# Performance work log

Hardware: AMD Instinct MI355X
Metric: run time of the kernel (lower is better)

The kernel has to match this reference:

```python
import jax, jax.numpy as jnp
import numpy as np

N, S, C, P, K = 64, 64, 128, 32, 1000   # batch, frames, in_planes, part_num, class_num
HPG = (3 * C) // 16                      # hidden channels per group for part_score mlp = 24
EPS = 1e-5


def setup_inputs() -> dict:
    key = jax.random.key(0)
    ks = jax.random.split(key, 8)
    return {
        "t_f": jax.random.normal(ks[0], (N, S, C, P), jnp.float32),
        "t_s": jax.random.normal(ks[1], (N, S, C, P), jnp.float32),
        "t_l": jax.random.normal(ks[2], (N, S, C, P), jnp.float32),
        # part_score grouped 1x1 convs (groups=P): per-group (out, in)
        "w1": jax.random.normal(ks[3], (P, HPG, 3 * C), jnp.float32) * 0.05,
        "bn1_gamma": jnp.ones((P, HPG), jnp.float32),
        "bn1_beta": jnp.zeros((P, HPG), jnp.float32),
        "w2": jax.random.normal(ks[4], (P, 1, HPG), jnp.float32) * 0.05,
        # decay_channel grouped 1x1 conv: per-group 3C -> C
        "wd": jax.random.normal(ks[5], (P, C, 3 * C), jnp.float32) * 0.05,
        # per-part BatchNorm1d(C) affine params
        "bn_gamma": jnp.ones((P, C), jnp.float32),
        "bn_beta": jnp.zeros((P, C), jnp.float32),
        # fc: (1, C, K) in torch; squeeze leading 1
        "fc": jax.random.normal(ks[6], (C, K), jnp.float32) * 0.05,
    }


def reference(t_f, t_s, t_l, w1, bn1_gamma, bn1_beta, w2, wd, bn_gamma, bn_beta, fc):
    # cat along channel dim then arrange as (n, p, 3c, s) == grouped conv layout
    x = jnp.concatenate([t_f, t_s, t_l], axis=2).transpose(0, 3, 2, 1)  # (n,p,3c,s)

    # --- part_score: grouped 1x1 conv -> BN (batch stats over n,s) -> LeakyReLU -> grouped conv -> sigmoid
    h = jnp.einsum('npis,poi->npos', x, w1)               # (n,p,HPG,s)
    mu = h.mean(axis=(0, 3), keepdims=True)
    var = h.var(axis=(0, 3), keepdims=True)               # biased var (torch training BN)
    h = (h - mu) / jnp.sqrt(var + EPS) * bn1_gamma[None, :, :, None] + bn1_beta[None, :, :, None]
    h = jnp.where(h >= 0, h, 0.01 * h)                    # LeakyReLU(0.01)
    score = jax.nn.sigmoid(jnp.einsum('npis,poi->npos', h, w2))  # (n,p,1,s)

    # --- decay_channel grouped 1x1 conv: 3c -> c per part
    feat = jnp.einsum('npis,poi->npos', x, wd)            # (n,p,c,s)

    # attention-weighted temporal pooling
    wpv = (feat * score).sum(-1) / score.sum(-1)          # (n,p,c)

    # per-part BatchNorm1d over batch dim (training-mode batch stats)
    m = wpv.mean(axis=0)                                  # (p,c)
    v = wpv.var(axis=0)
    part_feature = ((wpv - m) / jnp.sqrt(v + EPS) * bn_gamma + bn_beta).transpose(1, 0, 2)  # (p,n,c)

    part_classification = jnp.einsum('pnc,ck->pnk', part_feature, fc)  # (p,n,K)

    # argmax frame per (n,p) and gather from t_f
    idx = jnp.argmax(score[:, :, 0, :], axis=-1)          # (n,p)
    tfp = t_f.transpose(0, 3, 1, 2)                       # (n,p,s,c)
    selected = jnp.take_along_axis(tfp, idx[:, :, None, None], axis=2)[:, :, 0, :]  # (n,p,c)
    selected_part_feature = selected.transpose(1, 0, 2)   # (p,n,c)

    weighted_part_vector = wpv.transpose(1, 0, 2)         # (p,n,c)
    return part_classification, weighted_part_vector, selected_part_feature
```

## Files before the change

### kernel.cpp

```cpp
#include <hip/hip_runtime.h>
#include <math.h>

#define N 64
#define S 64
#define C 128
#define P 32
#define KCLS 1000
#define HPG 24
#define C3 384
#define NS 4096
#define EPSV 1e-5f

#define WS_H    0
#define WS_W1Z  (WS_H + P*HPG*NS)
#define WS_BNP  (WS_W1Z + 384*8*32*4)
#define WS_BNSS (WS_BNP + 512*768*2)
#define WS_Y    (WS_BNSS + P*HPG*2)
#define WS_Z    (WS_Y + P*N*C3)
#define WS_PF   (WS_Z + P*N)
#define WS_SC   (WS_PF + P*C*N)
#define WS_MI   (WS_SC + N*P*S)

__global__ __launch_bounds__(256) void k0w_w1z(
    const float* __restrict__ w1, float* __restrict__ w1z)
{
  int e = blockIdx.x * 256 + threadIdx.x;
  int p = e & 31;
  int og = (e >> 5) & 7;
  int i = e >> 8;
  float4 v;
  v.x = w1[(p * HPG + og * 3 + 0) * C3 + i];
  v.y = w1[(p * HPG + og * 3 + 1) * C3 + i];
  v.z = w1[(p * HPG + og * 3 + 2) * C3 + i];
  v.w = 0.f;
  ((float4*)w1z)[e] = v;
}

__global__ __launch_bounds__(256) void k01_h(
    const float* __restrict__ tf, const float* __restrict__ ts,
    const float* __restrict__ tl, const float* __restrict__ w1z,
    float* __restrict__ h, float* __restrict__ bnpT)
{
  int n = blockIdx.x, st = blockIdx.y;
  int s0 = st * 8;
  int t = threadIdx.x;
  int p = t & 31;
  int og = t >> 5;
  __shared__ float xl[8 * 1024];
  float acc[3][8];
  #pragma unroll
  for (int oo = 0; oo < 3; ++oo)
    #pragma unroll
    for (int s = 0; s < 8; ++s) acc[oo][s] = 0.f;

  const float4* w4p = (const float4*)w1z;
  const float* xp = &xl[p];
  for (int ch = 0; ch < 12; ++ch) {
    int z = ch >> 2, c0 = (ch & 3) * 32;
    const float* src = (z == 0) ? tf : (z == 1) ? ts : tl;
    const float* base = src + ((size_t)(n * S + s0)) * C * P + c0 * P;
    if (ch) __syncthreads();
    #pragma unroll
    for (int j = 0; j < 8; ++j) {
      int e = t + 256 * j;
      int s_loc = e >> 8;
      int idx = e & 255;
      float4 v = *(const float4*)&base[(size_t)s_loc * C * P + idx * 4];
      *(float4*)&xl[s_loc * 1024 + idx * 4] = v;
    }
    __syncthreads();
    #pragma unroll 4
    for (int cl = 0; cl < 32; ++cl) {
      int i = ch * 32 + cl;
      float4 w = w4p[(i * 8 + og) * 32 + p];
      float xs[8];
      #pragma unroll
      for (int s = 0; s < 8; ++s) xs[s] = xp[s * 1024 + cl * 32];
      #pragma unroll
      for (int s = 0; s < 8; ++s) {
        acc[0][s] += w.x * xs[s];
        acc[1][s] += w.y * xs[s];
        acc[2][s] += w.z * xs[s];
      }
    }
  }
  int nst = n * 8 + st;
  #pragma unroll
  for (int oo = 0; oo < 3; ++oo) {
    int o = og * 3 + oo;
    float* hp = h + (size_t)(p * HPG + o) * NS + n * S + s0;
    *(float4*)&hp[0] = make_float4(acc[oo][0], acc[oo][1], acc[oo][2], acc[oo][3]);
    *(float4*)&hp[4] = make_float4(acc[oo][4], acc[oo][5], acc[oo][6], acc[oo][7]);
    float sm = 0.f, sq = 0.f;
    #pragma unroll
    for (int s = 0; s < 8; ++s) { sm += acc[oo][s]; sq += acc[oo][s] * acc[oo][s]; }
    bnpT[(size_t)((p * HPG + o) * 2 + 0) * 512 + nst] = sm;
    bnpT[(size_t)((p * HPG + o) * 2 + 1) * 512 + nst] = sq;
  }
}

__global__ __launch_bounds__(256) void k2_bnstat(const float* __restrict__ bnpT,
    const float* __restrict__ g, const float* __restrict__ b,
    float* __restrict__ bnss)
{
  int blk = blockIdx.x;
  int t = threadIdx.x;
  int rl = t >> 4, lane = t & 15;
  int row = blk * 16 + rl;
  const float* rp = bnpT + (size_t)row * 512;
  float sm = 0.f;
  #pragma unroll 8
  for (int j = 0; j < 32; ++j) sm += rp[lane + 16 * j];
  __shared__ float red[16][17];
  red[rl][lane] = sm;
  __syncthreads();
  if (t < 16) {
    float s = 0.f;
    #pragma unroll
    for (int j = 0; j < 16; ++j) s += red[t][j];
    red[t][16] = s;
  }
  __syncthreads();
  if (t < 8) {
    int po = blk * 8 + t;
    float sum = red[t * 2][16];
    float sq  = red[t * 2 + 1][16];
    float mu  = sum / (float)NS;
    float var = sq / (float)NS - mu * mu;
    float sc = g[po] * rsqrtf(var + EPSV);
    bnss[po * 2]     = sc;
    bnss[po * 2 + 1] = b[po] - mu * sc;
  }
}

__global__ __launch_bounds__(256) void k3a_score(
    const float* __restrict__ h, const float* __restrict__ bnss,
    const float* __restrict__ w2,
    float* __restrict__ score, float* __restrict__ z,
    int* __restrict__ mi_out)
{
  int n = blockIdx.x;
  int p = blockIdx.y * 4 + (threadIdx.x >> 6);
  int l = threadIdx.x & 63;
  float ssum = 0.f;
  const float* hp = h + (size_t)p * HPG * NS + n * S;
  #pragma unroll
  for (int o = 0; o < HPG; ++o) {
    float hv = hp[(size_t)o * NS + l];
    float sc = bnss[(p * HPG + o) * 2];
    float sh = bnss[(p * HPG + o) * 2 + 1];
    float v = hv * sc + sh;
    v = (v >= 0.f) ? v : 0.01f * v;
    ssum += w2[p * HPG + o] * v;
  }
  float scr = 1.f / (1.f + expf(-ssum));
  float zs = scr;
  #pragma unroll
  for (int m = 1; m < 64; m <<= 1) zs += __shfl_xor(zs, m, 64);
  float mv = scr; int mi = l;
  #pragma unroll
  for (int m = 1; m < 64; m <<= 1) {
    float ov = __shfl_xor(mv, m, 64);
    int   oi = __shfl_xor(mi, m, 64);
    if (ov > mv || (ov == mv && oi < mi)) { mv = ov; mi = oi; }
  }
  if (l == 0) { z[p * N + n] = zs; mi_out[n * P + p] = mi; }
  score[((size_t)n * P + p) * S + l] = scr;
}

__global__ __launch_bounds__(256) void k3b_y(
    const float* __restrict__ tf, const float* __restrict__ ts,
    const float* __restrict__ tl, const float* __restrict__ score,
    const int* __restrict__ mi, float* __restrict__ y,
    float* __restrict__ out_spf)
{
  int n = blockIdx.x, chunk = blockIdx.y;
  int z = chunk >> 2, c0 = (chunk & 3) * 32;
  const float* src = (z == 0) ? tf : (z == 1) ? ts : tl;
  int t = threadIdx.x;
  int p = t & 31, cl = t >> 5;
  __shared__ float sc_lds[S * P];
  __shared__ int mi_lds[P];
  #pragma unroll
  for (int j = 0; j < 8; ++j) {
    int e = t + 256 * j;
    int s2 = e >> 5, pp = e & 31;
    sc_lds[s2 * P + pp] = score[((size_t)n * P + pp) * S + s2];
  }
  if (t < P) mi_lds[t] = mi[n * P + t];
  __syncthreads();
  int mymi = mi_lds[p];
  const float* base = src + (size_t)n * S * C * P + (size_t)(c0 + cl) * P + p;
  float acc[4] = {0.f, 0.f, 0.f, 0.f};
  float sel[4] = {0.f, 0.f, 0.f, 0.f};
  #pragma unroll 8
  for (int s = 0; s < S; ++s) {
    float scv = sc_lds[s * P + p];
    #pragma unroll
    for (int j = 0; j < 4; ++j) {
      float v = base[(size_t)s * C * P + j * 8 * P];
      acc[j] += v * scv;
      sel[j] = (s == mymi) ? v : sel[j];
    }
  }
  float* yp = y + ((size_t)p * N + n) * C3 + z * C + c0 + cl;
  #pragma unroll
  for (int j = 0; j < 4; ++j) yp[j * 8] = acc[j];
  if (z == 0) {
    float* sp = out_spf + ((size_t)p * N + n) * C + c0 + cl;
    #pragma unroll
    for (int j = 0; j < 4; ++j) sp[j * 8] = sel[j];
  }
}

__global__ __launch_bounds__(256) void k4_wpv(
    const float* __restrict__ y, const float* __restrict__ z,
    const float* __restrict__ wd, const float* __restrict__ g,
    const float* __restrict__ b, float* __restrict__ out_wpv,
    float* __restrict__ pf)
{
  int p   = blockIdx.x;
  int cch = blockIdx.y;
  int t = threadIdx.x;
  int n = t & 63, cg = t >> 6;
  int cbase = cch * 16 + cg * 4;
  __shared__ float ych[96][66];
  float acc[4] = {0.f, 0.f, 0.f, 0.f};
  const float* yp  = y  + (size_t)p * N * C3;
  const float* wdp = wd + (size_t)p * C * C3;
  for (int ch = 0; ch < 4; ++ch) {
    __syncthreads();
    #pragma unroll
    for (int j = 0; j < 24; ++j) {
      int e = t + 256 * j;
      int i = e % 96, nn = e / 96;
      ych[i][nn] = yp[nn * C3 + ch * 96 + i];
    }
    __syncthreads();
    #pragma unroll
    for (int sub = 0; sub < 4; ++sub) {
      float yr[24];
      #pragma unroll
      for (int kk = 0; kk < 24; ++kk) yr[kk] = ych[sub * 24 + kk][n];
      int ibase = ch * 96 + sub * 24;
      #pragma unroll
      for (int cl = 0; cl < 4; ++cl) {
        const float4* w4 = (const float4*)(wdp + (size_t)(cbase + cl) * C3 + ibase);
        float a = 0.f;
        #pragma unroll
        for (int q = 0; q < 6; ++q) {
          float4 wv = w4[q];
          a += yr[q*4+0] * wv.x + yr[q*4+1] * wv.y
             + yr[q*4+2] * wv.z + yr[q*4+3] * wv.w;
        }
        acc[cl] += a;
      }
    }
  }
  float zinv = 1.f / z[p * N + n];
  #pragma unroll
  for (int cl = 0; cl < 4; ++cl) acc[cl] *= zinv;
  #pragma unroll
  for (int cl = 0; cl < 4; ++cl) {
    float v = acc[cl];
    float s = v, q = v * v;
    #pragma unroll
    for (int m = 1; m < 64; m <<= 1) {
      s += __shfl_xor(s, m, 64);
      q += __shfl_xor(q, m, 64);
    }
    float mu  = s * (1.f / 64.f);
    float var = q * (1.f / 64.f) - mu * mu;
    int c = cbase + cl;
    float sc = g[p * C + c] * rsqrtf(var + EPSV);
    float sh = b[p * C + c] - mu * sc;
    pf[((size_t)p * C + c) * N + n] = v * sc + sh;
  }
  float4 wout = make_float4(acc[0], acc[1], acc[2], acc[3]);
  *(float4*)(out_wpv + ((size_t)p * N + n) * C + cbase) = wout;
}

__global__ __launch_bounds__(256) void k5_fc(
    const float* __restrict__ pf, const float* __restrict__ fc,
    float* __restrict__ out0)
{
  int kt = blockIdx.x;
  int p  = blockIdx.y;
  int n0 = blockIdx.z * 16;
  int t = threadIdx.x;
  int k = kt * 256 + t;
  bool ok = k < KCLS;
  int kk = ok ? k : (KCLS - 1);
  float acc[16];
  #pragma unroll
  for (int j = 0; j < 16; ++j) acc[j] = 0.f;
  for (int c = 0; c < C; ++c) {
    float fv = fc[c * KCLS + kk];
    const float4* row4 = (const float4*)(pf + ((size_t)p * C + c) * N + n0);
    #pragma unroll
    for (int j4 = 0; j4 < 4; ++j4) {
      float4 r = row4[j4];
      acc[j4*4+0] += r.x * fv; acc[j4*4+1] += r.y * fv;
      acc[j4*4+2] += r.z * fv; acc[j4*4+3] += r.w * fv;
    }
  }
  if (ok) {
    #pragma unroll 4
    for (int j = 0; j < 16; ++j)
      out0[(size_t)(p * N + n0 + j) * KCLS + k] = acc[j];
  }
}

extern "C" void kernel_launch(void* const* d_in, const int* in_sizes, int n_in,
                              void* d_out, int out_size, void* d_ws, size_t ws_size,
                              hipStream_t stream)
{
  const float* tf = (const float*)d_in[0];
  const float* ts = (const float*)d_in[1];
  const float* tl = (const float*)d_in[2];
  const float* w1 = (const float*)d_in[3];
  const float* g1 = (const float*)d_in[4];
  const float* b1 = (const float*)d_in[5];
  const float* w2 = (const float*)d_in[6];
  const float* wd = (const float*)d_in[7];
  const float* g  = (const float*)d_in[8];
  const float* b  = (const float*)d_in[9];
  const float* fc = (const float*)d_in[10];

  float* ws   = (float*)d_ws;
  float* h    = ws + WS_H;
  float* w1z  = ws + WS_W1Z;
  float* bnpT = ws + WS_BNP;
  float* bnss = ws + WS_BNSS;
  float* y    = ws + WS_Y;
  float* z    = ws + WS_Z;
  float* pf   = ws + WS_PF;
  float* sc   = ws + WS_SC;
  int*   mi   = (int*)(ws + WS_MI);

  float* out0 = (float*)d_out;
  float* out1 = out0 + P * N * KCLS;
  float* out2 = out1 + P * N * C;

  k0w_w1z<<<384, 256, 0, stream>>>(w1, w1z);
  k01_h<<<dim3(64, 8), 256, 0, stream>>>(tf, ts, tl, w1z, h, bnpT);
  k2_bnstat<<<96, 256, 0, stream>>>(bnpT, g1, b1, bnss);
  k3a_score<<<dim3(64, 8), 256, 0, stream>>>(h, bnss, w2, sc, z, mi);
  k3b_y<<<dim3(64, 12), 256, 0, stream>>>(tf, ts, tl, sc, mi, y, out2);
  k4_wpv<<<dim3(32, 8), 256, 0, stream>>>(y, z, wd, g, b, out1, pf);
  k5_fc<<<dim3(4, 32, 4), 256, 0, stream>>>(pf, fc, out0);
}
```

Before: 168.6 us.

## Split h-projection reduction across two blocks and compute BN stats from partial sums

The first grouped-conv kernel now splits the 384-channel reduction into two halves over a new grid dimension, doubling the block count from 512 to 1024 for better occupancy on the many-CU GPU. Each half writes its own partial h buffer, and the downstream BN-stat and score kernels add the two partials on read. The per-block sum/sumsq partials are dropped, so BN statistics are now computed by rereading the full h (twice, since both partials are read) with 768 blocks. This trades extra memory traffic for more parallelism in the projection stage.

After: 163.1 us. 3.3% less time.

```diff
diff --git a/kernel.cpp b/kernel.cpp
--- a/kernel.cpp
+++ b/kernel.cpp
@@ -12,9 +12,8 @@
 #define EPSV 1e-5f
 
 #define WS_H    0
-#define WS_W1Z  (WS_H + P*HPG*NS)
-#define WS_BNP  (WS_W1Z + 384*8*32*4)
-#define WS_BNSS (WS_BNP + 512*768*2)
+#define WS_W1Z  (WS_H + 2*P*HPG*NS)
+#define WS_BNSS (WS_W1Z + 384*8*32*4)
 #define WS_Y    (WS_BNSS + P*HPG*2)
 #define WS_Z    (WS_Y + P*N*C3)
 #define WS_PF   (WS_Z + P*N)
@@ -39,9 +38,9 @@
 __global__ __launch_bounds__(256) void k01_h(
     const float* __restrict__ tf, const float* __restrict__ ts,
     const float* __restrict__ tl, const float* __restrict__ w1z,
-    float* __restrict__ h, float* __restrict__ bnpT)
-{
-  int n = blockIdx.x, st = blockIdx.y;
+    float* __restrict__ h)
+{
+  int n = blockIdx.x, st = blockIdx.y, split = blockIdx.z;
   int s0 = st * 8;
   int t = threadIdx.x;
   int p = t & 31;
@@ -54,11 +53,13 @@
     for (int s = 0; s < 8; ++s) acc[oo][s] = 0.f;
 
   const float4* w4p = (const float4*)w1z;
+  const float* srcs[3] = {tf, ts, tl};
   const float* xp = &xl[p];
-  for (int ch = 0; ch < 12; ++ch) {
-    int z = ch >> 2, c0 = (ch & 3) * 32;
-    const float* src = (z == 0) ? tf : (z == 1) ? ts : tl;
-    const float* base = src + ((size_t)(n * S + s0)) * C * P + c0 * P;
+
+  for (int ch = 0; ch < 6; ++ch) {
+    int gch = split * 6 + ch;
+    int z = gch >> 2, c0 = (gch & 3) * 32;
+    const float* base = srcs[z] + ((size_t)(n * S + s0)) * C * P + c0 * P;
     if (ch) __syncthreads();
     #pragma unroll
     for (int j = 0; j < 8; ++j) {
@@ -71,7 +72,7 @@
     __syncthreads();
     #pragma unroll 4
     for (int cl = 0; cl < 32; ++cl) {
-      int i = ch * 32 + cl;
+      int i = gch * 32 + cl;
       float4 w = w4p[(i * 8 + og) * 32 + p];
       float xs[8];
       #pragma unroll
@@ -84,49 +85,46 @@
       }
     }
   }
-  int nst = n * 8 + st;
   #pragma unroll
   for (int oo = 0; oo < 3; ++oo) {
     int o = og * 3 + oo;
-    float* hp = h + (size_t)(p * HPG + o) * NS + n * S + s0;
+    float* hp = h + ((size_t)split * P * HPG + p * HPG + o) * NS + n * S + s0;
     *(float4*)&hp[0] = make_float4(acc[oo][0], acc[oo][1], acc[oo][2], acc[oo][3]);
     *(float4*)&hp[4] = make_float4(acc[oo][4], acc[oo][5], acc[oo][6], acc[oo][7]);
-    float sm = 0.f, sq = 0.f;
-    #pragma unroll
-    for (int s = 0; s < 8; ++s) { sm += acc[oo][s]; sq += acc[oo][s] * acc[oo][s]; }
-    bnpT[(size_t)((p * HPG + o) * 2 + 0) * 512 + nst] = sm;
-    bnpT[(size_t)((p * HPG + o) * 2 + 1) * 512 + nst] = sq;
-  }
-}
-
-__global__ __launch_bounds__(256) void k2_bnstat(const float* __restrict__ bnpT,
+  }
+}
+
+__global__ __launch_bounds__(256) void k2_bnstat(const float* __restrict__ h,
     const float* __restrict__ g, const float* __restrict__ b,
     float* __restrict__ bnss)
 {
-  int blk = blockIdx.x;
-  int t = threadIdx.x;
-  int rl = t >> 4, lane = t & 15;
-  int row = blk * 16 + rl;
-  const float* rp = bnpT + (size_t)row * 512;
-  float sm = 0.f;
-  #pragma unroll 8
-  for (int j = 0; j < 32; ++j) sm += rp[lane + 16 * j];
-  __shared__ float red[16][17];
-  red[rl][lane] = sm;
+  int po = blockIdx.x;
+  int t = threadIdx.x;
+  const float4* r0 = (const float4*)(h + (size_t)po * NS);
+  const float4* r1 = (const float4*)(h + (size_t)(P * HPG + po) * NS);
+  float sm = 0.f, sq = 0.f;
+  #pragma unroll
+  for (int k = 0; k < 4; ++k) {
+    float4 a = r0[t + 256 * k];
+    float4 c = r1[t + 256 * k];
+    float v0 = a.x + c.x, v1 = a.y + c.y, v2 = a.z + c.z, v3 = a.w + c.w;
+    sm += v0 + v1 + v2 + v3;
+    sq += v0 * v0 + v1 * v1 + v2 * v2 + v3 * v3;
+  }
+  #pragma unroll
+  for (int m = 1; m < 64; m <<= 1) {
+    sm += __shfl_xor(sm, m, 64);
+    sq += __shfl_xor(sq, m, 64);
+  }
+  __shared__ float red[4][2];
+  int w = t >> 6;
+  if ((t & 63) == 0) { red[w][0] = sm; red[w][1] = sq; }
   __syncthreads();
-  if (t < 16) {
-    float s = 0.f;
-    #pragma unroll
-    for (int j = 0; j < 16; ++j) s += red[t][j];
-    red[t][16] = s;
-  }
-  __syncthreads();
-  if (t < 8) {
-    int po = blk * 8 + t;
-    float sum = red[t * 2][16];
-    float sq  = red[t * 2 + 1][16];
+  if (t == 0) {
+    float sum = red[0][0] + red[1][0] + red[2][0] + red[3][0];
+    float ssq = red[0][1] + red[1][1] + red[2][1] + red[3][1];
     float mu  = sum / (float)NS;
-    float var = sq / (float)NS - mu * mu;
+    float var = ssq / (float)NS - mu * mu;
     float sc = g[po] * rsqrtf(var + EPSV);
     bnss[po * 2]     = sc;
     bnss[po * 2 + 1] = b[po] - mu * sc;
@@ -143,10 +141,11 @@
   int p = blockIdx.y * 4 + (threadIdx.x >> 6);
   int l = threadIdx.x & 63;
   float ssum = 0.f;
-  const float* hp = h + (size_t)p * HPG * NS + n * S;
+  const float* hp0 = h + (size_t)p * HPG * NS + n * S;
+  const float* hp1 = hp0 + (size_t)P * HPG * NS;
   #pragma unroll
   for (int o = 0; o < HPG; ++o) {
-    float hv = hp[(size_t)o * NS + l];
+    float hv = hp0[(size_t)o * NS + l] + hp1[(size_t)o * NS + l];
     float sc = bnss[(p * HPG + o) * 2];
     float sh = bnss[(p * HPG + o) * 2 + 1];
     float v = hv * sc + sh;
@@ -330,7 +329,6 @@
   float* ws   = (float*)d_ws;
   float* h    = ws + WS_H;
   float* w1z  = ws + WS_W1Z;
-  float* bnpT = ws + WS_BNP;
   float* bnss = ws + WS_BNSS;
   float* y    = ws + WS_Y;
   float* z    = ws + WS_Z;
@@ -343,8 +341,8 @@
   float* out2 = out1 + P * N * C;
 
   k0w_w1z<<<384, 256, 0, stream>>>(w1, w1z);
-  k01_h<<<dim3(64, 8), 256, 0, stream>>>(tf, ts, tl, w1z, h, bnpT);
-  k2_bnstat<<<96, 256, 0, stream>>>(bnpT, g1, b1, bnss);
+  k01_h<<<dim3(64, 8, 2), 256, 0, stream>>>(tf, ts, tl, w1z, h);
+  k2_bnstat<<<768, 256, 0, stream>>>(h, g1, b1, bnss);
   k3a_score<<<dim3(64, 8), 256, 0, stream>>>(h, bnss, w2, sc, z, mi);
   k3b_y<<<dim3(64, 12), 256, 0, stream>>>(tf, ts, tl, sc, mi, y, out2);
   k4_wpv<<<dim3(32, 8), 256, 0, stream>>>(y, z, wd, g, b, out1, pf);
```
